# Optimization experiments

Measured on AMD Instinct MI355X. Metric: run time of the kernel, lower is better.

The kernel has to match this reference:

```python
import math
import jax, jax.numpy as jnp
import numpy as np

B, L, ENC_IN, D_MODEL, D_FF, E_LAYERS, N_HEADS, FACTOR = 4, 2048, 32, 512, 2048, 2, 8, 5


def layer_norm(x, g, b, eps=1e-5):
    mu = jnp.mean(x, axis=-1, keepdims=True)
    var = jnp.mean((x - mu) ** 2, axis=-1, keepdims=True)
    return (x - mu) / jnp.sqrt(var + eps) * g + b


def positional_encoding(length, d_model):
    pos = np.arange(length, dtype=np.float32)[:, None]
    div = np.exp(np.arange(0, d_model, 2, dtype=np.float32) * -(math.log(10000.0) / d_model))
    pe = np.zeros((length, d_model), dtype=np.float32)
    pe[:, 0::2] = np.sin(pos * div)
    pe[:, 1::2] = np.cos(pos * div)
    return jnp.asarray(pe)


def circ_conv1d(x, w, b=None):
    # x: [B,L,Cin], w: [Cout,Cin,3]; kernel 3, circular padding 1, stride 1 -> [B,L,Cout]
    xc = jnp.transpose(x, (0, 2, 1))
    xc = jnp.pad(xc, ((0, 0), (0, 0), (1, 1)), mode='wrap')
    y = jax.lax.conv_general_dilated(xc, w, (1,), 'VALID',
                                     dimension_numbers=('NCH', 'OIH', 'NCH'))
    if b is not None:
        y = y + b[None, :, None]
    return jnp.transpose(y, (0, 2, 1))


def prob_attention(Q, K, V, key):
    # Q,K,V: [B,H,L,D]; ProbAttention(mask_flag=False, factor=5)
    Bq, H, Lq, D = Q.shape
    sample_k = min(FACTOR * int(math.ceil(math.log(Lq))), Lq)  # U_part
    n_top = min(FACTOR * int(math.ceil(math.log(Lq))), Lq)    # u
    idx = jax.random.randint(key, (Lq, sample_k), 0, Lq)
    K_samp = K[:, :, idx, :]                                  # [B,H,L,sample_k,D]
    QK_samp = jnp.einsum('bhld,bhlud->bhlu', Q, K_samp)
    M = QK_samp.max(axis=-1) - QK_samp.sum(axis=-1) / Lq      # sparsity measure [B,H,L]
    _, M_top = jax.lax.top_k(M, n_top)                        # [B,H,u]
    Q_red = jnp.take_along_axis(Q, M_top[..., None], axis=2)  # [B,H,u,D]
    scores = jnp.einsum('bhud,bhkd->bhuk', Q_red, K) / math.sqrt(D)
    attn = jax.nn.softmax(scores, axis=-1)
    upd = jnp.einsum('bhuk,bhkd->bhud', attn, V)
    # initial context = mean of V (mask_flag=False), overwritten at top-u rows
    ctx = jnp.broadcast_to(jnp.mean(V, axis=2, keepdims=True), (Bq, H, Lq, D))
    bi = jnp.arange(Bq)[:, None, None]
    hi = jnp.arange(H)[None, :, None]
    return ctx.at[bi, hi, M_top].set(upd)


def attention_layer(x, Wq, bq, Wk, bk, Wv, bv, Wo, bo, key):
    Bx, Lx, dm = x.shape
    D = dm // N_HEADS
    def split(h):
        return h.reshape(Bx, Lx, N_HEADS, D).transpose(0, 2, 1, 3)
    q = split(x @ Wq.T + bq)
    k = split(x @ Wk.T + bk)
    v = split(x @ Wv.T + bv)
    ctx = prob_attention(q, k, v, key)
    ctx = ctx.transpose(0, 2, 1, 3).reshape(Bx, Lx, dm)
    return ctx @ Wo.T + bo


def encoder_layer(x, Wq, bq, Wk, bk, Wv, bv, Wo, bo, W1, b1, W2, b2, g1, be1, g2, be2, key):
    x = x + attention_layer(x, Wq, bq, Wk, bk, Wv, bv, Wo, bo, key)
    x = layer_norm(x, g1, be1)
    y = jax.nn.gelu(x @ W1.T + b1, approximate=False)  # conv1 (kernel 1) + gelu
    y = y @ W2.T + b2                                  # conv2 (kernel 1)
    return layer_norm(x + y, g2, be2)


def conv_distil(x, w, b, bn_g, bn_b):
    y = circ_conv1d(x, w, b)
    mu = jnp.mean(y, axis=(0, 1))                      # BatchNorm1d (training-mode stats)
    var = jnp.mean((y - mu) ** 2, axis=(0, 1))
    y = (y - mu) / jnp.sqrt(var + 1e-5) * bn_g + bn_b
    y = jax.nn.elu(y)
    yt = jnp.transpose(y, (0, 2, 1))                   # MaxPool1d(k=3, s=2, p=1)
    yt = jax.lax.reduce_window(yt, -jnp.inf, jax.lax.max,
                               (1, 1, 3), (1, 1, 2), [(0, 0), (0, 0), (1, 1)])
    return jnp.transpose(yt, (0, 2, 1))


def setup_inputs() -> dict:
    key = jax.random.key(0)
    ks = iter(jax.random.split(key, 32))
    def nrm(shape, sc=0.02):
        return jax.random.normal(next(ks), shape, jnp.float32) * sc
    return {
        'x_enc': jax.random.normal(next(ks), (B, L, ENC_IN), jnp.float32),
        'tok_w': nrm((D_MODEL, ENC_IN, 3), 0.1),
        'Wq': nrm((E_LAYERS, D_MODEL, D_MODEL)), 'bq': jnp.zeros((E_LAYERS, D_MODEL)),
        'Wk': nrm((E_LAYERS, D_MODEL, D_MODEL)), 'bk': jnp.zeros((E_LAYERS, D_MODEL)),
        'Wv': nrm((E_LAYERS, D_MODEL, D_MODEL)), 'bv': jnp.zeros((E_LAYERS, D_MODEL)),
        'Wo': nrm((E_LAYERS, D_MODEL, D_MODEL)), 'bo': jnp.zeros((E_LAYERS, D_MODEL)),
        'W1': nrm((E_LAYERS, D_FF, D_MODEL)), 'b1': jnp.zeros((E_LAYERS, D_FF)),
        'W2': nrm((E_LAYERS, D_MODEL, D_FF)), 'b2': jnp.zeros((E_LAYERS, D_MODEL)),
        'ln1_g': jnp.ones((E_LAYERS, D_MODEL)), 'ln1_b': jnp.zeros((E_LAYERS, D_MODEL)),
        'ln2_g': jnp.ones((E_LAYERS, D_MODEL)), 'ln2_b': jnp.zeros((E_LAYERS, D_MODEL)),
        'conv_w': nrm((D_MODEL, D_MODEL, 3)), 'conv_b': jnp.zeros((D_MODEL,)),
        'bn_g': jnp.ones((D_MODEL,)), 'bn_b': jnp.zeros((D_MODEL,)),
        'normf_g': jnp.ones((D_MODEL,)), 'normf_b': jnp.zeros((D_MODEL,)),
        'proj_w': nrm((ENC_IN, D_MODEL)), 'proj_b': jnp.zeros((ENC_IN,)),
    }


def reference(x_enc, tok_w, Wq, bq, Wk, bk, Wv, bv, Wo, bo, W1, b1, W2, b2,
              ln1_g, ln1_b, ln2_g, ln2_b, conv_w, conv_b, bn_g, bn_b,
              normf_g, normf_b, proj_w, proj_b):
    keys = jax.random.split(jax.random.key(42), E_LAYERS)
    # DataEmbedding: circular token conv (no bias) + sinusoidal positional embedding
    x = circ_conv1d(x_enc, tok_w) + positional_encoding(x_enc.shape[1], D_MODEL)[None]
    for i in range(E_LAYERS):
        x = encoder_layer(x, Wq[i], bq[i], Wk[i], bk[i], Wv[i], bv[i], Wo[i], bo[i],
                          W1[i], b1[i], W2[i], b2[i],
                          ln1_g[i], ln1_b[i], ln2_g[i], ln2_b[i], keys[i])
        if i == 0:  # single distillation ConvLayer after first encoder layer
            x = conv_distil(x, conv_w, conv_b, bn_g, bn_b)
    x = layer_norm(x, normf_g, normf_b)
    out = x @ proj_w.T + proj_b
    return out[:, :L]  # [:, :seq_len] slice (no-op after distillation halves length)
```

## Files before the change

### kernel.cpp

```cpp
#include <hip/hip_runtime.h>
#include <cstdint>
#include <cmath>


#define NB 4
#define DM 512
#define NH 8
#define HD 64
#define QS 1536

typedef unsigned short ushort_t;
typedef __bf16 bf16x8 __attribute__((ext_vector_type(8)));
typedef float floatx4 __attribute__((ext_vector_type(4)));
typedef unsigned short ushort8_t __attribute__((ext_vector_type(8)));

__device__ inline ushort_t f2b(float f) {
  uint32_t u = __float_as_uint(f);
  uint32_t r = (u + 0x7fffu + ((u >> 16) & 1u)) >> 16;
  return (ushort_t)r;
}
__device__ inline float b2f(ushort_t u) {
  return __uint_as_float((uint32_t)u << 16);
}

__global__ void castqkv_k(const float* __restrict__ Wq,
                          const float* __restrict__ Wk,
                          const float* __restrict__ Wv,
                          ushort_t* __restrict__ out) {
  int gid = blockIdx.x * 256 + threadIdx.x;
  if (gid >= 393216) return;
  int ly = gid / 196608, r4 = gid - ly * 196608;
  int r = r4 >> 7, c4 = r4 & 127;
  int sel = r >> 9, srow = r & 511;
  const float* src = (sel == 0 ? Wq : sel == 1 ? Wk : Wv) + ly * 262144 +
                     srow * 512 + c4 * 4;
  float4 v = *(const float4*)src;
  ushort4 o;
  o.x = f2b(v.x); o.y = f2b(v.y); o.z = f2b(v.z); o.w = f2b(v.w);
  ((ushort4*)out)[ly * 196608 + r * 128 + c4] = o;
}

__global__ void castw3_k(const float* __restrict__ Wo,
                         const float* __restrict__ W1,
                         const float* __restrict__ W2,
                         const float* __restrict__ tw,
                         ushort_t* __restrict__ oWo, ushort_t* __restrict__ oW1,
                         ushort_t* __restrict__ oW2, ushort_t* __restrict__ otw) {
  int gid = blockIdx.x * 256 + threadIdx.x;
  if (gid >= 1191936) return;
  const float* src;
  ushort4* dst;
  int i;
  if (gid < 131072) { src = Wo; dst = (ushort4*)oWo; i = gid; }
  else if (gid < 655360) { src = W1; dst = (ushort4*)oW1; i = gid - 131072; }
  else if (gid < 1179648) { src = W2; dst = (ushort4*)oW2; i = gid - 655360; }
  else { src = tw; dst = (ushort4*)otw; i = gid - 1179648; }
  float4 v = ((const float4*)src)[i];
  ushort4 o;
  o.x = f2b(v.x); o.y = f2b(v.y); o.z = f2b(v.z); o.w = f2b(v.w);
  dst[i] = o;
}

__global__ void castw_conv_k(const float* __restrict__ in,
                             ushort_t* __restrict__ out) {
  int gid = blockIdx.x * 256 + threadIdx.x;
  int d = gid / 1536, r = gid - d * 1536;
  int t = r >> 9, i = r & 511;
  out[gid] = f2b(in[d * 1536 + i * 3 + t]);
}

__global__ void setup_small_k(const float* __restrict__ bq,
                              const float* __restrict__ bk,
                              const float* __restrict__ bv,
                              float* __restrict__ ZB,
                              float* __restrict__ BQKV) {
  int gid = blockIdx.x * 256 + threadIdx.x;
  if (gid >= 3584) return;
  if (gid < 512) { ZB[gid] = 0.f; return; }
  int g = gid - 512;
  int layer = g / 1536, r = g - layer * 1536;
  float v;
  if (r < 512) v = bq[layer * 512 + r];
  else if (r < 1024) v = bk[layer * 512 + r - 512];
  else v = bv[layer * 512 + r - 1024];
  BQKV[g] = v;
}

__host__ __device__ inline void threefry2x32(uint32_t k0, uint32_t k1,
                                             uint32_t c0, uint32_t c1,
                                             uint32_t* o0, uint32_t* o1) {
  uint32_t ks0 = k0, ks1 = k1, ks2 = k0 ^ k1 ^ 0x1BD11BDAu;
  uint32_t x0 = c0 + ks0;
  uint32_t x1 = c1 + ks1;
  const uint32_t rotA[4] = {13u, 15u, 26u, 6u};
  const uint32_t rotB[4] = {17u, 29u, 16u, 24u};
  uint32_t ks[3] = {ks0, ks1, ks2};
  #pragma unroll
  for (int i = 0; i < 5; ++i) {
    const uint32_t* r = (i & 1) ? rotB : rotA;
    #pragma unroll
    for (int j = 0; j < 4; ++j) {
      x0 += x1;
      x1 = (x1 << r[j]) | (x1 >> (32u - r[j]));
      x1 ^= x0;
    }
    x0 += ks[(i + 1) % 3];
    x1 += ks[(i + 2) % 3] + (uint32_t)(i + 1);
  }
  *o0 = x0; *o1 = x1;
}

__global__ void gen_idx_k(int* __restrict__ idx, int n, int mask,
                          uint32_t k0, uint32_t k1) {
  int i = blockIdx.x * 256 + threadIdx.x;
  if (i < n) {
    uint32_t o0, o1;
    threefry2x32(k0, k1, 0u, (uint32_t)i, &o0, &o1);
    idx[i] = (int)((o0 ^ o1) & (uint32_t)mask);
  }
}

__device__ inline float wave_sum64(float v) {
  #pragma unroll
  for (int o = 32; o > 0; o >>= 1) v += __shfl_xor(v, o, 64);
  return v;
}

__global__ void pe_k(float* __restrict__ pe) {
  int i = blockIdx.x * 256 + threadIdx.x;
  int d = i & 511, l = i >> 9;
  int j2 = d & ~1;
  float div = expf((float)j2 * -1.7988946039e-2f);
  float ang = (float)l * div;
  pe[i] = (d & 1) ? cosf(ang) : sinf(ang);
}

__global__ void im2col_tok_k(const float* __restrict__ xe,
                             ushort_t* __restrict__ A) {
  int gid = blockIdx.x * 256 + threadIdx.x;
  int col = gid % 96;
  int row = gid / 96;
  int c = col / 3, t = col - c * 3;
  int b = row >> 11, l = row & 2047;
  int ls = (l + t - 1) & 2047;
  A[gid] = f2b(xe[((size_t)b * 2048 + ls) * 32 + c]);
}

__device__ inline void gload16(const ushort_t* g, ushort_t* l) {
  __builtin_amdgcn_global_load_lds(
      (const __attribute__((address_space(1))) unsigned int*)(const void*)g,
      (__attribute__((address_space(3))) unsigned int*)(void*)l, 16, 0, 0);
}

template <int CONV, int GELU, int OMODE, int ADDPE>
__global__ __launch_bounds__(512) void mgemm_k(
    const ushort_t* __restrict__ A, const ushort_t* __restrict__ W,
    const float* __restrict__ bias, float* __restrict__ Cf,
    ushort_t* __restrict__ Cb, const float* __restrict__ pe,
    int X, int ldc, int K) {
  __shared__ ushort_t As[128 * 32];
  __shared__ ushort_t Bs[128 * 32];
  int id = blockIdx.x;
  int cc = id & 7, j = id >> 3;
  int bx = j % X;
  int by = (j / X) * 8 + cc;
  int m0 = by * 128, n0 = bx * 128;
  int t = threadIdx.x;
  int lane = t & 63, wv = t >> 6;
  int rl = lane >> 2, cl = (lane & 3) * 8;
  int Ra = wv * 16;
  int ga_row = m0 + Ra + rl;
  const ushort_t* gA = A + (size_t)ga_row * K + cl;
  const ushort_t* gB = W + (size_t)(n0 + Ra + rl) * K + cl;
  ushort_t* lA = As + Ra * 32;
  ushort_t* lB = Bs + Ra * 32;
  int cb = ga_row >> 11, clr = ga_row & 2047;

  int quad = lane >> 4, lr = lane & 15;
  int wm = wv >> 1, wn = wv & 1;

  floatx4 acc[2][4] = {};
  for (int ks = 0; ks < K; ks += 32) {
    if (ks) __syncthreads();
    if (CONV) {
      int tt = ks >> 9;
      int c = (ks & 511) + cl;
      int ls = (clr + tt - 1) & 2047;
      gload16(A + ((size_t)(cb * 2048 + ls) * 512 + c), lA);
    } else {
      gload16(gA, lA);
      gA += 32;
    }
    gload16(gB, lB);
    gB += 32;
    __syncthreads();
    bf16x8 av[2], bv[4];
    #pragma unroll
    for (int mt = 0; mt < 2; ++mt)
      av[mt] = *(const bf16x8*)&As[(wm * 32 + mt * 16 + lr) * 32 + quad * 8];
    #pragma unroll
    for (int nt = 0; nt < 4; ++nt)
      bv[nt] = *(const bf16x8*)&Bs[(wn * 64 + nt * 16 + lr) * 32 + quad * 8];
    #pragma unroll
    for (int mt = 0; mt < 2; ++mt)
      #pragma unroll
      for (int nt = 0; nt < 4; ++nt)
        acc[mt][nt] = __builtin_amdgcn_mfma_f32_16x16x32_bf16(
            av[mt], bv[nt], acc[mt][nt], 0, 0, 0);
  }
  #pragma unroll
  for (int nt = 0; nt < 4; ++nt) {
    int col = n0 + wn * 64 + nt * 16 + lr;
    float bsv = bias[col];
    #pragma unroll
    for (int mt = 0; mt < 2; ++mt) {
      int row0 = m0 + wm * 32 + mt * 16 + quad * 4;
      #pragma unroll
      for (int r = 0; r < 4; ++r) {
        int row = row0 + r;
        float v = acc[mt][nt][r] + bsv;
        if (ADDPE) v += pe[(size_t)(row & 2047) * ldc + col];
        if (GELU) v = 0.5f * v * (1.0f + erff(v * 0.70710678118654752f));
        if (OMODE == 0 || OMODE == 2) Cf[(size_t)row * ldc + col] = v;
        if (OMODE == 1 || OMODE == 2) Cb[(size_t)row * ldc + col] = f2b(v);
      }
    }
  }
}

__global__ __launch_bounds__(256) void gemm_k(
    const float* __restrict__ A, const float* __restrict__ W,
    const float* __restrict__ bias, float* __restrict__ C,
    int M, int N, int K) {
  __shared__ float As2[16][64 + 4];
  __shared__ float Ws2[16][64 + 4];
  int m0 = blockIdx.y * 64, n0 = blockIdx.x * 64;
  int t = threadIdx.x;
  int tx = t & 15, ty = t >> 4;
  float acc[4][4] = {};
  for (int k0 = 0; k0 < K; k0 += 16) {
    #pragma unroll
    for (int i = 0; i < 4; ++i) {
      int li = t + i * 256;
      int m = li >> 4, kk = li & 15;
      As2[kk][m] = A[(size_t)(m0 + m) * K + k0 + kk];
    }
    #pragma unroll
    for (int i = 0; i < 4; ++i) {
      int li = t + i * 256;
      int n = li >> 4, kk = li & 15;
      int gn = n0 + n;
      Ws2[kk][n] = (gn < N) ? W[(size_t)gn * K + k0 + kk] : 0.0f;
    }
    __syncthreads();
    #pragma unroll
    for (int kk = 0; kk < 16; ++kk) {
      float4 avv = *(const float4*)&As2[kk][ty * 4];
      float4 bvv = *(const float4*)&Ws2[kk][tx * 4];
      float a[4] = {avv.x, avv.y, avv.z, avv.w};
      float bb[4] = {bvv.x, bvv.y, bvv.z, bvv.w};
      #pragma unroll
      for (int i = 0; i < 4; ++i)
        #pragma unroll
        for (int j = 0; j < 4; ++j) acc[i][j] += a[i] * bb[j];
    }
    __syncthreads();
  }
  #pragma unroll
  for (int i = 0; i < 4; ++i) {
    int m = m0 + ty * 4 + i;
    #pragma unroll
    for (int j = 0; j < 4; ++j) {
      int n = n0 + tx * 4 + j;
      if (n < N) C[(size_t)m * N + n] = acc[i][j] + bias[n];
    }
  }
}

__global__ __launch_bounds__(128) void ln_k(
    const float* __restrict__ A, const float* __restrict__ Bres,
    const float* __restrict__ g, const float* __restrict__ be,
    float* __restrict__ O, ushort_t* __restrict__ Ob) {
  int r = blockIdx.x, t = threadIdx.x;
  __shared__ float lds[2];
  float4 v = ((const float4*)(A + (size_t)r * DM))[t];
  if (Bres) {
    float4 u = ((const float4*)(Bres + (size_t)r * DM))[t];
    v.x += u.x; v.y += u.y; v.z += u.z; v.w += u.w;
  }
  float s = wave_sum64(v.x + v.y + v.z + v.w);
  int w = t >> 6;
  if ((t & 63) == 0) lds[w] = s;
  __syncthreads();
  float mu = (lds[0] + lds[1]) * (1.0f / 512.0f);
  __syncthreads();
  float dx = v.x - mu, dy = v.y - mu, dz = v.z - mu, dw = v.w - mu;
  float sq = wave_sum64(dx * dx + dy * dy + dz * dz + dw * dw);
  if ((t & 63) == 0) lds[w] = sq;
  __syncthreads();
  float var = (lds[0] + lds[1]) * (1.0f / 512.0f);
  float inv = 1.0f / sqrtf(var + 1e-5f);
  float4 gv = ((const float4*)g)[t];
  float4 bv = ((const float4*)be)[t];
  float4 o;
  o.x = dx * inv * gv.x + bv.x;
  o.y = dy * inv * gv.y + bv.y;
  o.z = dz * inv * gv.z + bv.z;
  o.w = dw * inv * gv.w + bv.w;
  ((float4*)(O + (size_t)r * DM))[t] = o;
  if (Ob) {
    ushort4 ob;
    ob.x = f2b(o.x); ob.y = f2b(o.y); ob.z = f2b(o.z); ob.w = f2b(o.w);
    ((ushort4*)(Ob + (size_t)r * DM))[t] = ob;
  }
}

template <int UU>
__global__ __launch_bounds__(256) void qk_m_k(
    const ushort_t* __restrict__ QKVb, const int* __restrict__ idx,
    float* __restrict__ Mout, int Lx) {
  int l = blockIdx.x;
  int b = threadIdx.x >> 6;
  int lane = threadIdx.x & 63;
  const ushort_t* qp = QKVb + ((size_t)b * Lx + l) * QS + lane * 8;
  float q[8];
  {
    ushort8_t qv = *(const ushort8_t*)qp;
    #pragma unroll
    for (int c = 0; c < 8; ++c) q[c] = b2f(qv[c]);
  }
  const ushort_t* Kbase = QKVb + (size_t)b * Lx * QS + 512 + lane * 8;
  const int* ip = idx + (size_t)l * UU;
  float maxv = -INFINITY, sumv = 0.f;
  #pragma unroll
  for (int u0 = 0; u0 < UU; u0 += 8) {
    ushort8_t kv[8];
    #pragma unroll
    for (int j = 0; j < 8; ++j) {
      if (u0 + j < UU)
        kv[j] = *(const ushort8_t*)(Kbase + (size_t)ip[u0 + j] * QS);
    }
    #pragma unroll
    for (int j = 0; j < 8; ++j) {
      if (u0 + j < UU) {
        float p = 0.f;
        #pragma unroll
        for (int c = 0; c < 8; ++c) p += q[c] * b2f(kv[j][c]);
        p += __shfl_xor(p, 1, 64);
        p += __shfl_xor(p, 2, 64);
        p += __shfl_xor(p, 4, 64);
        maxv = fmaxf(maxv, p);
        sumv += p;
      }
    }
  }
  if ((lane & 7) == 0) {
    int h = lane >> 3;
    Mout[(size_t)(b * 8 + h) * Lx + l] = maxv - sumv / (float)Lx;
  }
}

__global__ __launch_bounds__(1024) void topk_k(
    const float* __restrict__ Mbuf, int* __restrict__ Mtop, int Lx, int U) {
  int nch = Lx >> 8;
  int bh = blockIdx.x / nch, ch = blockIdx.x % nch;
  const float* m = Mbuf + (size_t)bh * Lx;
  __shared__ float sm[2048];
  __shared__ int part[1024];
  int t = threadIdx.x;
  int c = t & 255, q = t >> 8;
  for (int i = t; i < Lx; i += 1024) sm[i] = m[i];
  __syncthreads();
  int i0 = (ch << 8) + c;
  float v0 = sm[i0];
  int r0 = 0;
  int qlen = Lx >> 2;
  int j0 = q * qlen, j1 = j0 + qlen;
  for (int j = j0; j < j1; j += 4) {
    float4 mj = *(const float4*)&sm[j];
    r0 += (mj.x > v0) || (mj.x == v0 && (j + 0) < i0);
    r0 += (mj.y > v0) || (mj.y == v0 && (j + 1) < i0);
    r0 += (mj.z > v0) || (mj.z == v0 && (j + 2) < i0);
    r0 += (mj.w > v0) || (mj.w == v0 && (j + 3) < i0);
  }
  part[t] = r0;
  __syncthreads();
  if (q == 0) {
    int r = part[c] + part[c + 256] + part[c + 512] + part[c + 768];
    if (r < U) Mtop[bh * U + r] = i0;
  }
}

__global__ __launch_bounds__(512) void meanv1_k(const ushort_t* __restrict__ QKVb,
                                                float* __restrict__ part,
                                                int Lx) {
  int b = blockIdx.x >> 4, chunk = blockIdx.x & 15;
  int rows = Lx >> 4;
  int t = threadIdx.x;
  const ushort_t* vp =
      QKVb + ((size_t)b * Lx + (size_t)chunk * rows) * QS + 1024 + t;
  float s = 0.f;
  for (int l = 0; l < rows; ++l) s += b2f(vp[(size_t)l * QS]);
  part[(size_t)blockIdx.x * DM + t] = s;
}
__global__ __launch_bounds__(512) void meanv2_k(const float* __restrict__ part,
                                                float* __restrict__ mv,
                                                int Lx) {
  int b = blockIdx.x, t = threadIdx.x;
  float s = 0.f;
  #pragma unroll
  for (int c = 0; c < 16; ++c) s += part[(size_t)(b * 16 + c) * DM + t];
  mv[b * DM + t] = s / (float)Lx;
}

__global__ void fillctx_k(ushort_t* __restrict__ ctx,
                          const float* __restrict__ mv, int Lx) {
  size_t i4 = (size_t)blockIdx.x * 256 + threadIdx.x;
  int col4 = (int)(i4 & 127);
  size_t row = i4 >> 7;
  int b = (int)(row / (size_t)Lx);
  const float* m = mv + b * DM + col4 * 4;
  ushort4 o;
  o.x = f2b(m[0]); o.y = f2b(m[1]); o.z = f2b(m[2]); o.w = f2b(m[3]);
  ((ushort4*)ctx)[i4] = o;
}

template <int UP>
__global__ __launch_bounds__(256) void attn_mfma_k(
    const ushort_t* __restrict__ QKVb, const int* __restrict__ Mtop,
    float* __restrict__ part, int Lx, int U, int nblk) {
  __shared__ ushort_t Ps[4][UP * 72];
  __shared__ ushort_t Vs[4][64 * 64];
  int bh = blockIdx.x / nblk, blkc = blockIdx.x % nblk;
  int h = bh & 7, b = bh >> 3;
  int t = threadIdx.x;
  int wv = t >> 6, lane = t & 63;
  int quad = lane >> 4, lr = lane & 15;
  int chunk = blkc * 4 + wv;
  int k0 = chunk * 64;
  const ushort_t* Qb = QKVb + (size_t)b * Lx * QS + h * HD;
  const ushort_t* Kb = Qb + 512;
  const ushort_t* Vb = Qb + 1024;

  bf16x8 qf[3][2];
  #pragma unroll
  for (int mt = 0; mt < 3; ++mt) {
    int u = mt * 16 + lr;
    int qi = Mtop[bh * U + (u < U ? u : U - 1)];
    const ushort_t* qp = Qb + (size_t)qi * QS + quad * 8;
    qf[mt][0] = *(const bf16x8*)qp;
    qf[mt][1] = *(const bf16x8*)(qp + 32);
  }

  ushort_t* vs = Vs[wv];
  #pragma unroll
  for (int i = 0; i < 8; ++i) {
    int cid = i * 64 + lane;
    int k = cid >> 3, c = cid & 7;
    ushort8_t v = *(const ushort8_t*)(Vb + (size_t)(k0 + k) * QS + c * 8);
    *(ushort8_t*)&vs[k * 64 + ((c * 8) ^ (((k >> 3) & 3) << 4))] = v;
  }

  floatx4 Sa[3][4] = {};
  #pragma unroll
  for (int kt = 0; kt < 4; ++kt) {
    const ushort_t* kp = Kb + (size_t)(k0 + kt * 16 + lr) * QS + quad * 8;
    bf16x8 kf0 = *(const bf16x8*)kp;
    bf16x8 kf1 = *(const bf16x8*)(kp + 32);
    #pragma unroll
    for (int mt = 0; mt < 3; ++mt) {
      Sa[mt][kt] = __builtin_amdgcn_mfma_f32_16x16x32_bf16(
          qf[mt][0], kf0, Sa[mt][kt], 0, 0, 0);
      Sa[mt][kt] = __builtin_amdgcn_mfma_f32_16x16x32_bf16(
          qf[mt][1], kf1, Sa[mt][kt], 0, 0, 0);
    }
  }

  float m_[3][4], l_[3][4];
  #pragma unroll
  for (int mt = 0; mt < 3; ++mt) {
    #pragma unroll
    for (int kt = 0; kt < 4; ++kt) Sa[mt][kt] *= 0.125f;
    #pragma unroll
    for (int r = 0; r < 4; ++r) {
      float mx = fmaxf(fmaxf(Sa[mt][0][r], Sa[mt][1][r]),
                       fmaxf(Sa[mt][2][r], Sa[mt][3][r]));
      #pragma unroll
      for (int o = 1; o <= 8; o <<= 1) mx = fmaxf(mx, __shfl_xor(mx, o, 64));
      float rs = 0.f;
      #pragma unroll
      for (int kt = 0; kt < 4; ++kt) {
        float e = __expf(Sa[mt][kt][r] - mx);
        Sa[mt][kt][r] = e;
        rs += e;
      }
      #pragma unroll
      for (int o = 1; o <= 8; o <<= 1) rs += __shfl_xor(rs, o, 64);
      m_[mt][r] = mx;
      l_[mt][r] = rs;
    }
  }

  ushort_t* ps = Ps[wv];
  floatx4 Oa[3][4] = {};
  #pragma unroll
  for (int pass = 0; pass < 2; ++pass) {
    #pragma unroll
    for (int mt = 0; mt < 3; ++mt)
      #pragma unroll
      for (int kt = 0; kt < 4; ++kt)
        #pragma unroll
        for (int r = 0; r < 4; ++r) {
          float e = Sa[mt][kt][r];
          ushort_t hb = f2b(e);
          ps[(mt * 16 + quad * 4 + r) * 72 + kt * 16 + lr] = hb;
          Sa[mt][kt][r] = e - b2f(hb);
        }
    #pragma unroll
    for (int kk = 0; kk < 2; ++kk) {
      bf16x8 pf[3];
      #pragma unroll
      for (int mt = 0; mt < 3; ++mt)
        pf[mt] = *(const bf16x8*)&ps[(mt * 16 + lr) * 72 + kk * 32 + quad * 8];
      #pragma unroll
      for (int nt = 0; nt < 4; ++nt) {
        ushort8_t vt;
        #pragma unroll
        for (int j = 0; j < 8; ++j)
          vt[j] = vs[(kk * 32 + quad * 8 + j) * 64 +
                     ((nt * 16 + lr) ^ (quad << 4))];
        bf16x8 vf = *(bf16x8*)&vt;
        #pragma unroll
        for (int mt = 0; mt < 3; ++mt)
          Oa[mt][nt] = __builtin_amdgcn_mfma_f32_16x16x32_bf16(
              pf[mt], vf, Oa[mt][nt], 0, 0, 0);
      }
    }
  }

  float* pb = part + (size_t)(bh * (nblk * 4) + chunk) * U * 66;
  #pragma unroll
  for (int mt = 0; mt < 3; ++mt) {
    #pragma unroll
    for (int r = 0; r < 4; ++r) {
      int u = mt * 16 + quad * 4 + r;
      if (u < U) {
        #pragma unroll
        for (int nt = 0; nt < 4; ++nt)
          pb[(size_t)u * 66 + nt * 16 + lr] = Oa[mt][nt][r];
        if (lr == 0) {
          pb[(size_t)u * 66 + 64] = m_[mt][r];
          pb[(size_t)u * 66 + 65] = l_[mt][r];
        }
      }
    }
  }
}

__global__ __launch_bounds__(64) void attn_merge_k(
    const float* __restrict__ part, const int* __restrict__ Mtop,
    ushort_t* __restrict__ ctx, int Lx, int U, int nchunk) {
  int bu = blockIdx.x;
  int u = bu % U, bh = bu / U;
  int h = bh & 7, b = bh >> 3;
  int d = threadIdx.x;
  float M = -INFINITY;
  for (int c = 0; c < nchunk; ++c)
    M = fmaxf(M, part[((size_t)(bh * nchunk + c) * U + u) * 66 + 64]);
  float L = 0.f, O = 0.f;
  for (int c = 0; c < nchunk; ++c) {
    const float* pp = part + ((size_t)(bh * nchunk + c) * U + u) * 66;
    float w = __expf(pp[64] - M);
    L += pp[65] * w;
    O += pp[d] * w;
  }
  int qi = Mtop[bh * U + u];
  ctx[((size_t)b * Lx + qi) * DM + h * HD + d] = f2b(O / L);
}

__global__ __launch_bounds__(256) void bn1_k(const float* __restrict__ Y,
                                             float* __restrict__ ps,
                                             float* __restrict__ pq) {
  int blk = blockIdx.x;
  int t = threadIdx.x;
  float s0 = 0, q0 = 0, s1 = 0, q1 = 0;
  const float* base = Y + (size_t)blk * 256 * DM;
  for (int r = 0; r < 256; ++r) {
    float a = base[(size_t)r * DM + t];
    float b = base[(size_t)r * DM + t + 256];
    s0 += a; q0 += a * a; s1 += b; q1 += b * b;
  }
  ps[blk * DM + t] = s0; ps[blk * DM + t + 256] = s1;
  pq[blk * DM + t] = q0; pq[blk * DM + t + 256] = q1;
}
__global__ __launch_bounds__(512) void bn2_k(const float* __restrict__ ps,
                                             const float* __restrict__ pq,
                                             float* __restrict__ mu,
                                             float* __restrict__ var) {
  int t = threadIdx.x;
  float s = 0, q = 0;
  #pragma unroll
  for (int c = 0; c < 32; ++c) { s += ps[c * DM + t]; q += pq[c * DM + t]; }
  float m = s * (1.0f / 8192.f);
  mu[t] = m;
  var[t] = q * (1.0f / 8192.f) - m * m;
}

__global__ void bnpool_k(const float* __restrict__ Y,
                         const float* __restrict__ mu,
                         const float* __restrict__ var,
                         const float* __restrict__ g,
                         const float* __restrict__ be, float* __restrict__ O,
                         ushort_t* __restrict__ Ob) {
  size_t i = (size_t)blockIdx.x * 256 + threadIdx.x;
  int c = (int)(i & 511);
  size_t row = i >> 9;
  int lo = (int)(row & 1023);
  int b = (int)(row >> 10);
  float sc = g[c] / sqrtf(var[c] + 1e-5f);
  float sh = be[c] - mu[c] * sc;
  int l0 = 2 * lo - 1;
  float m = -INFINITY;
  #pragma unroll
  for (int tt = 0; tt < 3; ++tt) {
    int l = l0 + tt;
    if (l >= 0 && l < 2048) {
      float v = Y[((size_t)b * 2048 + l) * DM + c] * sc + sh;
      v = v > 0.f ? v : expm1f(v);
      m = fmaxf(m, v);
    }
  }
  O[i] = m;
  Ob[i] = f2b(m);
}

extern "C" void kernel_launch(void* const* d_in, const int* in_sizes, int n_in,
                              void* d_out, int out_size, void* d_ws,
                              size_t ws_size, hipStream_t stream) {
  (void)in_sizes; (void)n_in; (void)out_size; (void)ws_size;
  const float* x_enc  = (const float*)d_in[0];
  const float* tok_w  = (const float*)d_in[1];
  const float* Wq     = (const float*)d_in[2];
  const float* bq     = (const float*)d_in[3];
  const float* Wk     = (const float*)d_in[4];
  const float* bk     = (const float*)d_in[5];
  const float* Wv     = (const float*)d_in[6];
  const float* bv     = (const float*)d_in[7];
  const float* Wo     = (const float*)d_in[8];
  const float* bo     = (const float*)d_in[9];
  const float* W1     = (const float*)d_in[10];
  const float* b1     = (const float*)d_in[11];
  const float* W2     = (const float*)d_in[12];
  const float* b2     = (const float*)d_in[13];
  const float* ln1_g  = (const float*)d_in[14];
  const float* ln1_b  = (const float*)d_in[15];
  const float* ln2_g  = (const float*)d_in[16];
  const float* ln2_b  = (const float*)d_in[17];
  const float* conv_w = (const float*)d_in[18];
  const float* conv_b = (const float*)d_in[19];
  const float* bn_g   = (const float*)d_in[20];
  const float* bn_b   = (const float*)d_in[21];
  const float* normf_g = (const float*)d_in[22];
  const float* normf_b = (const float*)d_in[23];
  const float* proj_w = (const float*)d_in[24];
  const float* proj_b = (const float*)d_in[25];
  float* out = (float*)d_out;
  float* ws = (float*)d_ws;

  float* X    = ws;
  float* SCR  = ws + 4194304;
  ushort_t* CTXb = (ushort_t*)(ws + 16777216);
  float* Y2   = ws + 20971520;
  float* Mb   = ws + 25165824;
  float* MV   = ws + 25231360;
  float* MVP  = ws + 25233408;
  float* BNps = ws + 25266176;
  float* BNpq = ws + 25282560;
  float* BNmu = ws + 25298944;
  float* BNvr = ws + 25299456;
  float* ZB   = ws + 25299968;
  float* BQKV = ws + 25300480;
  int*   IDX  = (int*)(ws + 25303552);
  int*   MT   = (int*)(ws + 25385472);
  ushort_t* U0   = (ushort_t*)(ws + 25386752);
  ushort_t* Xb   = U0;
  ushort_t* Hb   = U0 + 4194304;
  ushort_t* QKVb = Hb;
  ushort_t* Wqkvb= U0 + 20971520;
  ushort_t* Wob  = U0 + 22544384;
  ushort_t* W1b  = U0 + 23068672;
  ushort_t* W2b  = U0 + 25165824;
  ushort_t* Cwb  = U0 + 27262976;
  ushort_t* Twb  = U0 + 28049408;
  ushort_t* Atok = U0 + 28098560;
  float* PEf = ws + 39829248;

  castqkv_k<<<1536, 256, 0, stream>>>(Wq, Wk, Wv, Wqkvb);
  castw3_k<<<4656, 256, 0, stream>>>(Wo, W1, W2, tok_w, Wob, W1b, W2b, Twb);
  castw_conv_k<<<3072, 256, 0, stream>>>(conv_w, Cwb);
  setup_small_k<<<14, 256, 0, stream>>>(bq, bk, bv, ZB, BQKV);
  pe_k<<<4096, 256, 0, stream>>>(PEf);
  im2col_tok_k<<<3072, 256, 0, stream>>>(x_enc, Atok);

  mgemm_k<0, 0, 2, 1><<<256, 512, 0, stream>>>(
      Atok, Twb, ZB, X, Xb, PEf, 4, DM, 96);

  for (int layer = 0; layer < 2; ++layer) {
    const int Lx = (layer == 0) ? 2048 : 1024;
    const int U  = (layer == 0) ? 40 : 35;
    const int M  = NB * Lx;
    const int Yt = M / 128;
    const int NCHT = Lx / 64;
    const int NBLK = NCHT / 4;

    uint32_t kl0, kl1, s0, s1;
    threefry2x32(0u, 42u, 0u, (uint32_t)layer, &kl0, &kl1);
    threefry2x32(kl0, kl1, 0u, 1u, &s0, &s1);
    int nidx = Lx * U;
    gen_idx_k<<<(nidx + 255) / 256, 256, 0, stream>>>(IDX, nidx, Lx - 1, s0, s1);

    mgemm_k<0, 0, 1, 0><<<12 * Yt, 512, 0, stream>>>(
        Xb, Wqkvb + (size_t)layer * 786432, BQKV + layer * 1536, nullptr, QKVb,
        nullptr, 12, QS, DM);

    if (layer == 0)
      qk_m_k<40><<<Lx, 256, 0, stream>>>(QKVb, IDX, Mb, Lx);
    else
      qk_m_k<35><<<Lx, 256, 0, stream>>>(QKVb, IDX, Mb, Lx);
    topk_k<<<NB * NH * (Lx >> 8), 1024, 0, stream>>>(Mb, MT, Lx, U);
    meanv1_k<<<NB * 16, 512, 0, stream>>>(QKVb, MVP, Lx);
    meanv2_k<<<NB, 512, 0, stream>>>(MVP, MV, Lx);
    fillctx_k<<<(M * DM / 4) / 256, 256, 0, stream>>>(CTXb, MV, Lx);
    attn_mfma_k<48><<<NB * NH * NBLK, 256, 0, stream>>>(QKVb, MT, Y2, Lx, U,
                                                        NBLK);
    attn_merge_k<<<NB * NH * U, 64, 0, stream>>>(Y2, MT, CTXb, Lx, U, NCHT);

    mgemm_k<0, 0, 0, 0><<<4 * Yt, 512, 0, stream>>>(
        CTXb, Wob + (size_t)layer * 262144, bo + layer * DM, Y2, nullptr,
        nullptr, 4, DM, DM);
    ln_k<<<M, 128, 0, stream>>>(X, Y2, ln1_g + layer * DM, ln1_b + layer * DM, X, Xb);

    mgemm_k<0, 1, 1, 0><<<16 * Yt, 512, 0, stream>>>(
        Xb, W1b + (size_t)layer * 1048576, b1 + layer * 2048, nullptr, Hb,
        nullptr, 16, 2048, DM);
    mgemm_k<0, 0, 0, 0><<<4 * Yt, 512, 0, stream>>>(
        Hb, W2b + (size_t)layer * 1048576, b2 + layer * DM, Y2, nullptr,
        nullptr, 4, DM, 2048);
    ln_k<<<M, 128, 0, stream>>>(X, Y2, ln2_g + layer * DM, ln2_b + layer * DM, X, Xb);

    if (layer == 0) {
      mgemm_k<1, 0, 0, 0><<<4 * 64, 512, 0, stream>>>(
          Xb, Cwb, conv_b, Y2, nullptr, nullptr, 4, DM, 1536);
      bn1_k<<<32, 256, 0, stream>>>(Y2, BNps, BNpq);
      bn2_k<<<1, 512, 0, stream>>>(BNps, BNpq, BNmu, BNvr);
      bnpool_k<<<(NB * 1024 * 512) / 256, 256, 0, stream>>>(
          Y2, BNmu, BNvr, bn_g, bn_b, X, Xb);
    }
  }

  ln_k<<<NB * 1024, 128, 0, stream>>>(X, nullptr, normf_g, normf_b, SCR, nullptr);
  gemm_k<<<dim3(1, 4096 / 64), 256, 0, stream>>>(SCR, proj_w, proj_b, out,
                                                 4096, 32, DM);
}
```

Baseline: 680.8 us.

## Double-buffer GEMM LDS tiles and stage bf16 epilogue through shared memory

The MFMA GEMM now uses two LDS buffers so the global-to-LDS loads for the next K step are issued before the current step's MFMAs, with one barrier per iteration instead of two. For bf16 outputs, results are first written to a per-wave padded LDS tile and then stored as 16-byte vectors, replacing scattered 2-byte global stores. Shared memory use grows from 16 KB to 36 KB per block, which may lower occupancy.

```diff
diff --git a/kernel.cpp b/kernel.cpp
--- a/kernel.cpp
+++ b/kernel.cpp
@@ -158,8 +158,7 @@
     const float* __restrict__ bias, float* __restrict__ Cf,
     ushort_t* __restrict__ Cb, const float* __restrict__ pe,
     int X, int ldc, int K) {
-  __shared__ ushort_t As[128 * 32];
-  __shared__ ushort_t Bs[128 * 32];
+  __shared__ __align__(16) ushort_t SH[18432];
   int id = blockIdx.x;
   int cc = id & 7, j = id >> 3;
   int bx = j % X;
@@ -172,58 +171,103 @@
   int ga_row = m0 + Ra + rl;
   const ushort_t* gA = A + (size_t)ga_row * K + cl;
   const ushort_t* gB = W + (size_t)(n0 + Ra + rl) * K + cl;
-  ushort_t* lA = As + Ra * 32;
-  ushort_t* lB = Bs + Ra * 32;
   int cb = ga_row >> 11, clr = ga_row & 2047;
 
   int quad = lane >> 4, lr = lane & 15;
   int wm = wv >> 1, wn = wv & 1;
 
   floatx4 acc[2][4] = {};
-  for (int ks = 0; ks < K; ks += 32) {
-    if (ks) __syncthreads();
+  {
+    ushort_t* lA = SH + Ra * 32;
+    ushort_t* lB = SH + 4096 + Ra * 32;
     if (CONV) {
-      int tt = ks >> 9;
-      int c = (ks & 511) + cl;
-      int ls = (clr + tt - 1) & 2047;
-      gload16(A + ((size_t)(cb * 2048 + ls) * 512 + c), lA);
+      int ls = (clr - 1) & 2047;
+      gload16(A + ((size_t)(cb * 2048 + ls) * 512 + cl), lA);
     } else {
       gload16(gA, lA);
-      gA += 32;
     }
     gload16(gB, lB);
-    gB += 32;
-    __syncthreads();
+  }
+  __syncthreads();
+  int cur = 0;
+  for (int ks = 0; ks < K; ks += 32) {
+    int nxt = ks + 32;
+    if (nxt < K) {
+      ushort_t* lA = SH + (cur ^ 1) * 8192 + Ra * 32;
+      ushort_t* lB = lA + 4096;
+      if (CONV) {
+        int tt = nxt >> 9;
+        int c = (nxt & 511) + cl;
+        int ls = (clr + tt - 1) & 2047;
+        gload16(A + ((size_t)(cb * 2048 + ls) * 512 + c), lA);
+      } else {
+        gload16(gA + nxt, lA);
+      }
+      gload16(gB + nxt, lB);
+    }
+    const ushort_t* Ab = SH + cur * 8192;
+    const ushort_t* Bb = Ab + 4096;
     bf16x8 av[2], bv[4];
     #pragma unroll
     for (int mt = 0; mt < 2; ++mt)
-      av[mt] = *(const bf16x8*)&As[(wm * 32 + mt * 16 + lr) * 32 + quad * 8];
+      av[mt] = *(const bf16x8*)&Ab[(wm * 32 + mt * 16 + lr) * 32 + quad * 8];
     #pragma unroll
     for (int nt = 0; nt < 4; ++nt)
-      bv[nt] = *(const bf16x8*)&Bs[(wn * 64 + nt * 16 + lr) * 32 + quad * 8];
+      bv[nt] = *(const bf16x8*)&Bb[(wn * 64 + nt * 16 + lr) * 32 + quad * 8];
     #pragma unroll
     for (int mt = 0; mt < 2; ++mt)
       #pragma unroll
       for (int nt = 0; nt < 4; ++nt)
         acc[mt][nt] = __builtin_amdgcn_mfma_f32_16x16x32_bf16(
             av[mt], bv[nt], acc[mt][nt], 0, 0, 0);
-  }
-  #pragma unroll
-  for (int nt = 0; nt < 4; ++nt) {
-    int col = n0 + wn * 64 + nt * 16 + lr;
-    float bsv = bias[col];
-    #pragma unroll
-    for (int mt = 0; mt < 2; ++mt) {
-      int row0 = m0 + wm * 32 + mt * 16 + quad * 4;
-      #pragma unroll
-      for (int r = 0; r < 4; ++r) {
-        int row = row0 + r;
-        float v = acc[mt][nt][r] + bsv;
-        if (ADDPE) v += pe[(size_t)(row & 2047) * ldc + col];
-        if (GELU) v = 0.5f * v * (1.0f + erff(v * 0.70710678118654752f));
-        if (OMODE == 0 || OMODE == 2) Cf[(size_t)row * ldc + col] = v;
-        if (OMODE == 1 || OMODE == 2) Cb[(size_t)row * ldc + col] = f2b(v);
+    __syncthreads();
+    cur ^= 1;
+  }
+
+  if (OMODE == 0) {
+    #pragma unroll
+    for (int nt = 0; nt < 4; ++nt) {
+      int col = n0 + wn * 64 + nt * 16 + lr;
+      float bsv = bias[col];
+      #pragma unroll
+      for (int mt = 0; mt < 2; ++mt) {
+        int row0 = m0 + wm * 32 + mt * 16 + quad * 4;
+        #pragma unroll
+        for (int r = 0; r < 4; ++r) {
+          int row = row0 + r;
+          float v = acc[mt][nt][r] + bsv;
+          if (ADDPE) v += pe[(size_t)(row & 2047) * ldc + col];
+          if (GELU) v = 0.5f * v * (1.0f + erff(v * 0.70710678118654752f));
+          Cf[(size_t)row * ldc + col] = v;
+        }
       }
+    }
+  } else {
+    ushort_t* ep = SH + wv * 2304;
+    #pragma unroll
+    for (int nt = 0; nt < 4; ++nt) {
+      int col = n0 + wn * 64 + nt * 16 + lr;
+      float bsv = bias[col];
+      #pragma unroll
+      for (int mt = 0; mt < 2; ++mt) {
+        #pragma unroll
+        for (int r = 0; r < 4; ++r) {
+          int row = m0 + wm * 32 + mt * 16 + quad * 4 + r;
+          float v = acc[mt][nt][r] + bsv;
+          if (ADDPE) v += pe[(size_t)(row & 2047) * ldc + col];
+          if (GELU) v = 0.5f * v * (1.0f + erff(v * 0.70710678118654752f));
+          if (OMODE == 2) Cf[(size_t)row * ldc + col] = v;
+          ep[(mt * 16 + quad * 4 + r) * 72 + nt * 16 + lr] = f2b(v);
+        }
+      }
+    }
+    int r8 = lane >> 3, c8 = (lane & 7) * 8;
+    #pragma unroll
+    for (int i = 0; i < 4; ++i) {
+      int row = i * 8 + r8;
+      ushort8_t vv = *(const ushort8_t*)&ep[row * 72 + c8];
+      *(ushort8_t*)&Cb[(size_t)(m0 + wm * 32 + row) * ldc + n0 + wn * 64 + c8] =
+          vv;
     }
   }
 }
```

Measured after the change: 654.7 us. 3.8% less time.
